# Kernel tuning notes

Measured on AMD Instinct MI355X. Metric: run time of the kernel, lower is better.

## Reference

```python
import jax, jax.numpy as jnp
import numpy as np

NUM_SEGMENTS = 16


def setup_inputs() -> dict:
    key = jax.random.key(0)
    k1, k2, k3 = jax.random.split(key, 3)
    x = jax.random.normal(k1, (8, 128, 512, 512), dtype=jnp.float32)
    conv_w = jax.random.normal(k2, (NUM_SEGMENTS, 1, 3, 3), dtype=jnp.float32) * (1.0 / 3.0)
    conv_b = jax.random.normal(k3, (NUM_SEGMENTS,), dtype=jnp.float32) * 0.1
    return {"x": x, "conv_w": conv_w, "conv_b": conv_b}


def reference(x, conv_w, conv_b):
    nseg = conv_w.shape[0]
    S = int(np.sqrt(nseg))  # size_segments (grid is S x S)
    B, C, H, W = x.shape
    ws = H // S  # tile side
    # L2 norm over channel dim, keepdim -> [B,1,H,W]
    l2 = jnp.sqrt(jnp.sum(x * x, axis=1, keepdims=True))
    # Extract S*S tiles in row-major (i,j) order -> [B, nseg, ws, ws]
    tiles = l2.reshape(B, S, ws, S, ws).transpose(0, 1, 3, 2, 4).reshape(B, nseg, ws, ws)
    # One distinct 3x3 conv (1->1 ch, pad 1) per tile == grouped conv with nseg groups
    y = jax.lax.conv_general_dilated(
        tiles, conv_w,
        window_strides=(1, 1), padding="SAME",
        feature_group_count=nseg,
        dimension_numbers=("NCHW", "OIHW", "NCHW"),
    )
    y = jax.nn.sigmoid(y + conv_b[None, :, None, None])
    # torch: chunk along channel, cat along dim=2 -> [B,1,nseg*ws,ws], then .view(l2.shape)
    return y.reshape(B, 1, nseg * ws, ws).reshape(B, 1, H, W)
```

## Files before the change

### kernel.cpp

```cpp
#include <hip/hip_runtime.h>
#include <math.h>

#define B_    8
#define C_    128
#define H_    512
#define W_    512
#define HW_   (H_ * W_)
#define NSEG_ 16
#define TS_   128
#define SGRID_ 4

__global__ __launch_bounds__(256) void l2norm_kernel(const float* __restrict__ x,
                                                     float* __restrict__ l2) {
    int t = blockIdx.x * blockDim.x + threadIdx.x;
    int q = t << 2;
    int b = q >> 18;
    int hw = q & (HW_ - 1);
    const float* p = x + (size_t)b * C_ * HW_ + hw;
    float s0 = 0.f, s1 = 0.f, s2 = 0.f, s3 = 0.f;
#pragma unroll 8
    for (int c = 0; c < C_; ++c) {
        float4 v = *reinterpret_cast<const float4*>(p + (size_t)c * HW_);
        s0 = fmaf(v.x, v.x, s0);
        s1 = fmaf(v.y, v.y, s1);
        s2 = fmaf(v.z, v.z, s2);
        s3 = fmaf(v.w, v.w, s3);
    }
    float4 r;
    r.x = sqrtf(s0); r.y = sqrtf(s1); r.z = sqrtf(s2); r.w = sqrtf(s3);
    *reinterpret_cast<float4*>(l2 + q) = r;
}

__global__ __launch_bounds__(256) void tileconv_kernel(const float* __restrict__ l2,
                                                       const float* __restrict__ w,
                                                       const float* __restrict__ bias,
                                                       float* __restrict__ out) {
    int t = blockIdx.x * blockDim.x + threadIdx.x;
    int c   = t & (TS_ - 1);
    int r   = (t >> 7) & (TS_ - 1);
    int seg = (t >> 14) & (NSEG_ - 1);
    int b   = t >> 18;
    int ti = seg >> 2;
    int tj = seg & 3;

    const float* wp = w + seg * 9;
    float w00 = wp[0], w01 = wp[1], w02 = wp[2];
    float w10 = wp[3], w11 = wp[4], w12 = wp[5];
    float w20 = wp[6], w21 = wp[7], w22 = wp[8];

    const float* base = l2 + (size_t)b * HW_ + (size_t)(ti * TS_) * W_ + tj * TS_;

    float acc = bias[seg];
    bool up = (r > 0), dn = (r < TS_ - 1);
    bool lf = (c > 0), rt = (c < TS_ - 1);

    const float* row0 = base + (r - 1) * W_ + c;
    const float* row1 = row0 + W_;
    const float* row2 = row1 + W_;

    if (up) {
        if (lf) acc = fmaf(row0[-1], w00, acc);
        acc = fmaf(row0[0], w01, acc);
        if (rt) acc = fmaf(row0[1], w02, acc);
    }
    if (lf) acc = fmaf(row1[-1], w10, acc);
    acc = fmaf(row1[0], w11, acc);
    if (rt) acc = fmaf(row1[1], w12, acc);
    if (dn) {
        if (lf) acc = fmaf(row2[-1], w20, acc);
        acc = fmaf(row2[0], w21, acc);
        if (rt) acc = fmaf(row2[1], w22, acc);
    }

    out[t] = 1.0f / (1.0f + expf(-acc));
}

extern "C" void kernel_launch(void* const* d_in, const int* in_sizes, int n_in,
                              void* d_out, int out_size, void* d_ws, size_t ws_size,
                              hipStream_t stream) {
    const float* x      = (const float*)d_in[0];
    const float* conv_w = (const float*)d_in[1];
    const float* conv_b = (const float*)d_in[2];
    float* out = (float*)d_out;
    float* l2  = (float*)d_ws;

    int n1 = B_ * HW_ / 4;
    l2norm_kernel<<<n1 / 256, 256, 0, stream>>>(x, l2);

    int n2 = B_ * NSEG_ * TS_ * TS_;
    tileconv_kernel<<<n2 / 256, 256, 0, stream>>>(l2, conv_w, conv_b, out);
}
```

Baseline: 1.327 ms.

## Fuse channel L2 norm and per-tile 3x3 conv into one kernel with LDS halo

Replaces the two-kernel pipeline with a single kernel. Each block computes the L2 norm for a 16-row strip of one tile plus a one-row halo, stores it in shared memory, and then applies the 3x3 conv and sigmoid from there. This removes the global l2 round trip and one launch. In exchange, halo rows are recomputed, which adds roughly 12% extra reads of the dominant 1 GiB input. Channel iteration starts at a block-dependent offset to stagger memory access.

```diff
diff --git a/kernel.cpp b/kernel.cpp
--- a/kernel.cpp
+++ b/kernel.cpp
@@ -1,78 +1,121 @@
 #include <hip/hip_runtime.h>
 #include <math.h>
 
-#define B_    8
-#define C_    128
-#define H_    512
-#define W_    512
-#define HW_   (H_ * W_)
-#define NSEG_ 16
-#define TS_   128
-#define SGRID_ 4
+#define B_     8
+#define C_     128
+#define H_     512
+#define W_     512
+#define HW_    (H_ * W_)
+#define NSEG_  16
+#define TS_    128
+#define R_     16
+#define LROWS_ (R_ + 2)
+#define LSTR_  136
 
-__global__ __launch_bounds__(256) void l2norm_kernel(const float* __restrict__ x,
-                                                     float* __restrict__ l2) {
-    int t = blockIdx.x * blockDim.x + threadIdx.x;
-    int q = t << 2;
-    int b = q >> 18;
-    int hw = q & (HW_ - 1);
-    const float* p = x + (size_t)b * C_ * HW_ + hw;
-    float s0 = 0.f, s1 = 0.f, s2 = 0.f, s3 = 0.f;
-#pragma unroll 8
-    for (int c = 0; c < C_; ++c) {
-        float4 v = *reinterpret_cast<const float4*>(p + (size_t)c * HW_);
-        s0 = fmaf(v.x, v.x, s0);
-        s1 = fmaf(v.y, v.y, s1);
-        s2 = fmaf(v.z, v.z, s2);
-        s3 = fmaf(v.w, v.w, s3);
-    }
-    float4 r;
-    r.x = sqrtf(s0); r.y = sqrtf(s1); r.z = sqrtf(s2); r.w = sqrtf(s3);
-    *reinterpret_cast<float4*>(l2 + q) = r;
-}
+__global__ __launch_bounds__(256) void fused_kernel(const float* __restrict__ x,
+                                                    const float* __restrict__ w,
+                                                    const float* __restrict__ bias,
+                                                    float* __restrict__ out) {
+    __shared__ float l2s[LROWS_][LSTR_];
 
-__global__ __launch_bounds__(256) void tileconv_kernel(const float* __restrict__ l2,
-                                                       const float* __restrict__ w,
-                                                       const float* __restrict__ bias,
-                                                       float* __restrict__ out) {
-    int t = blockIdx.x * blockDim.x + threadIdx.x;
-    int c   = t & (TS_ - 1);
-    int r   = (t >> 7) & (TS_ - 1);
-    int seg = (t >> 14) & (NSEG_ - 1);
-    int b   = t >> 18;
-    int ti = seg >> 2;
-    int tj = seg & 3;
+    const int tid = threadIdx.x;
+    const int blk = blockIdx.x;
+    const int s   = blk & 7;
+    const int seg = (blk >> 3) & (NSEG_ - 1);
+    const int b   = blk >> 7;
+    const int ti  = seg >> 2;
+    const int tj  = seg & 3;
 
     const float* wp = w + seg * 9;
-    float w00 = wp[0], w01 = wp[1], w02 = wp[2];
-    float w10 = wp[3], w11 = wp[4], w12 = wp[5];
-    float w20 = wp[6], w21 = wp[7], w22 = wp[8];
+    const float w00 = wp[0], w01 = wp[1], w02 = wp[2];
+    const float w10 = wp[3], w11 = wp[4], w12 = wp[5];
+    const float w20 = wp[6], w21 = wp[7], w22 = wp[8];
+    const float bb  = bias[seg];
 
-    const float* base = l2 + (size_t)b * HW_ + (size_t)(ti * TS_) * W_ + tj * TS_;
+    if (tid < LROWS_) { l2s[tid][3] = 0.f; l2s[tid][4 + TS_] = 0.f; }
 
-    float acc = bias[seg];
-    bool up = (r > 0), dn = (r < TS_ - 1);
-    bool lf = (c > 0), rt = (c < TS_ - 1);
+    const int p0 = tid, p1 = tid + 256, p2 = tid + 512;
+    const int rr0 = p0 >> 5, rr1 = p1 >> 5, rr2 = p2 >> 5;
+    const int c40 = p0 & 31, c41 = p1 & 31, c42 = p2 & 31;
+    const bool have2 = (tid < 64);
 
-    const float* row0 = base + (r - 1) * W_ + c;
-    const float* row1 = row0 + W_;
-    const float* row2 = row1 + W_;
+    const int ht0 = s * R_ + rr0 - 1;
+    const int ht1 = s * R_ + rr1 - 1;
+    const int ht2 = s * R_ + rr2 - 1;
+    const bool rv0 = (ht0 >= 0);
+    const bool rv2 = (ht2 <= TS_ - 1);
+    const int hc0 = rv0 ? ht0 : 0;
+    const int hc2 = rv2 ? ht2 : TS_ - 1;
 
-    if (up) {
-        if (lf) acc = fmaf(row0[-1], w00, acc);
-        acc = fmaf(row0[0], w01, acc);
-        if (rt) acc = fmaf(row0[1], w02, acc);
-    }
-    if (lf) acc = fmaf(row1[-1], w10, acc);
-    acc = fmaf(row1[0], w11, acc);
-    if (rt) acc = fmaf(row1[1], w12, acc);
-    if (dn) {
-        if (lf) acc = fmaf(row2[-1], w20, acc);
-        acc = fmaf(row2[0], w21, acc);
-        if (rt) acc = fmaf(row2[1], w22, acc);
+    const size_t bbase = (size_t)b * C_ * HW_;
+    const int wbase = tj * TS_;
+    const int c0 = blk & (C_ - 1);
+
+    const float* q0 = x + bbase + (size_t)c0 * HW_ + (size_t)(ti * TS_ + hc0) * W_ + wbase + c40 * 4;
+    const float* q1 = x + bbase + (size_t)c0 * HW_ + (size_t)(ti * TS_ + ht1) * W_ + wbase + c41 * 4;
+    const float* q2 = x + bbase + (size_t)c0 * HW_ + (size_t)(ti * TS_ + hc2) * W_ + wbase + c42 * 4;
+
+    float4 a0 = make_float4(0.f, 0.f, 0.f, 0.f);
+    float4 a1 = make_float4(0.f, 0.f, 0.f, 0.f);
+    float4 a2 = make_float4(0.f, 0.f, 0.f, 0.f);
+
+#define BODY                                                                      \
+    {                                                                             \
+        float4 v0 = *reinterpret_cast<const float4*>(q0); q0 += HW_;              \
+        a0.x = fmaf(v0.x, v0.x, a0.x); a0.y = fmaf(v0.y, v0.y, a0.y);             \
+        a0.z = fmaf(v0.z, v0.z, a0.z); a0.w = fmaf(v0.w, v0.w, a0.w);             \
+        float4 v1 = *reinterpret_cast<const float4*>(q1); q1 += HW_;              \
+        a1.x = fmaf(v1.x, v1.x, a1.x); a1.y = fmaf(v1.y, v1.y, a1.y);             \
+        a1.z = fmaf(v1.z, v1.z, a1.z); a1.w = fmaf(v1.w, v1.w, a1.w);             \
+        if (have2) {                                                              \
+            float4 v2 = *reinterpret_cast<const float4*>(q2);                     \
+            a2.x = fmaf(v2.x, v2.x, a2.x); a2.y = fmaf(v2.y, v2.y, a2.y);         \
+            a2.z = fmaf(v2.z, v2.z, a2.z); a2.w = fmaf(v2.w, v2.w, a2.w);         \
+        }                                                                         \
+        q2 += HW_;                                                                \
     }
 
-    out[t] = 1.0f / (1.0f + expf(-acc));
+    const int n1 = C_ - c0;
+#pragma unroll 4
+    for (int i = 0; i < n1; ++i) BODY
+    q0 -= (size_t)C_ * HW_;
+    q1 -= (size_t)C_ * HW_;
+    q2 -= (size_t)C_ * HW_;
+#pragma unroll 4
+    for (int i = 0; i < c0; ++i) BODY
+#undef BODY
+
+    float4 r0v, r1v;
+    if (rv0) r0v = make_float4(sqrtf(a0.x), sqrtf(a0.y), sqrtf(a0.z), sqrtf(a0.w));
+    else     r0v = make_float4(0.f, 0.f, 0.f, 0.f);
+    r1v = make_float4(sqrtf(a1.x), sqrtf(a1.y), sqrtf(a1.z), sqrtf(a1.w));
+    *reinterpret_cast<float4*>(&l2s[rr0][4 + c40 * 4]) = r0v;
+    *reinterpret_cast<float4*>(&l2s[rr1][4 + c41 * 4]) = r1v;
+    if (have2) {
+        float4 r2v;
+        if (rv2) r2v = make_float4(sqrtf(a2.x), sqrtf(a2.y), sqrtf(a2.z), sqrtf(a2.w));
+        else     r2v = make_float4(0.f, 0.f, 0.f, 0.f);
+        *reinterpret_cast<float4*>(&l2s[rr2][4 + c42 * 4]) = r2v;
+    }
+
+    __syncthreads();
+
+    const int c  = tid & (TS_ - 1);
+    const int r2 = tid >> 7;
+    float* op = out + (((size_t)(b * NSEG_ + seg)) << 14) + ((size_t)(s * R_) << 7) + c;
+
+#pragma unroll
+    for (int k = 0; k < 8; ++k) {
+        const int r = r2 + 2 * k;
+        const float* L0 = &l2s[r    ][3 + c];
+        const float* L1 = &l2s[r + 1][3 + c];
+        const float* L2 = &l2s[r + 2][3 + c];
+        float acc = bb;
+        acc = fmaf(L0[0], w00, acc); acc = fmaf(L0[1], w01, acc); acc = fmaf(L0[2], w02, acc);
+        acc = fmaf(L1[0], w10, acc); acc = fmaf(L1[1], w11, acc); acc = fmaf(L1[2], w12, acc);
+        acc = fmaf(L2[0], w20, acc); acc = fmaf(L2[1], w21, acc); acc = fmaf(L2[2], w22, acc);
+        op[(size_t)r << 7] = 1.0f / (1.0f + expf(-acc));
+    }
 }
 
 extern "C" void kernel_launch(void* const* d_in, const int* in_sizes, int n_in,
@@ -82,11 +125,6 @@
     const float* conv_w = (const float*)d_in[1];
     const float* conv_b = (const float*)d_in[2];
     float* out = (float*)d_out;
-    float* l2  = (float*)d_ws;
 
-    int n1 = B_ * HW_ / 4;
-    l2norm_kernel<<<n1 / 256, 256, 0, stream>>>(x, l2);
-
-    int n2 = B_ * NSEG_ * TS_ * TS_;
-    tileconv_kernel<<<n2 / 256, 256, 0, stream>>>(l2, conv_w, conv_b, out);
+    fused_kernel<<<B_ * NSEG_ * 8, 256, 0, stream>>>(x, conv_w, conv_b, out);
 }
```

Result: slower. 1.378 ms (+3.8%).

## Process more pixels per thread and stagger channel start across blocks in L2 norm

Applied to the files above, without the earlier changes.

The L2-norm kernel now gives each thread 16 pixels (four float4 loads per channel), launching 512 blocks instead of 2048. Each block starts its channel loop at a different offset (blockIdx mod C) and wraps around. The staggering is meant to spread concurrent accesses across memory channels and avoid blocks hitting the same channel planes at once, and the wider per-thread work adds memory-level parallelism. The cost is fewer resident waves on the GPU, which could leave bandwidth unused.

```diff
diff --git a/kernel.cpp b/kernel.cpp
--- a/kernel.cpp
+++ b/kernel.cpp
@@ -1,34 +1,73 @@
 #include <hip/hip_runtime.h>
 #include <math.h>
 
-#define B_    8
-#define C_    128
-#define H_    512
-#define W_    512
-#define HW_   (H_ * W_)
-#define NSEG_ 16
-#define TS_   128
+#define B_     8
+#define C_     128
+#define H_     512
+#define W_     512
+#define HW_    (H_ * W_)
+#define NSEG_  16
+#define TS_    128
 #define SGRID_ 4
 
 __global__ __launch_bounds__(256) void l2norm_kernel(const float* __restrict__ x,
                                                      float* __restrict__ l2) {
-    int t = blockIdx.x * blockDim.x + threadIdx.x;
-    int q = t << 2;
-    int b = q >> 18;
-    int hw = q & (HW_ - 1);
-    const float* p = x + (size_t)b * C_ * HW_ + hw;
-    float s0 = 0.f, s1 = 0.f, s2 = 0.f, s3 = 0.f;
-#pragma unroll 8
-    for (int c = 0; c < C_; ++c) {
-        float4 v = *reinterpret_cast<const float4*>(p + (size_t)c * HW_);
-        s0 = fmaf(v.x, v.x, s0);
-        s1 = fmaf(v.y, v.y, s1);
-        s2 = fmaf(v.z, v.z, s2);
-        s3 = fmaf(v.w, v.w, s3);
+    const int tid = threadIdx.x;
+    const int blk = blockIdx.x;
+    const int px0 = blk << 12;
+    const int b   = px0 >> 18;
+    const int hw  = px0 & (HW_ - 1);
+
+    const float* base = x + (size_t)b * C_ * HW_ + hw;
+
+    float4 a0 = make_float4(0.f, 0.f, 0.f, 0.f);
+    float4 a1 = make_float4(0.f, 0.f, 0.f, 0.f);
+    float4 a2 = make_float4(0.f, 0.f, 0.f, 0.f);
+    float4 a3 = make_float4(0.f, 0.f, 0.f, 0.f);
+
+    const int c0 = blk & (C_ - 1);
+    const float* p = base + (size_t)c0 * HW_;
+
+    const int o0 = tid << 2;
+    const int o1 = o0 + 1024;
+    const int o2 = o0 + 2048;
+    const int o3 = o0 + 3072;
+
+#define BODY                                                                   \
+    {                                                                          \
+        float4 v0 = *reinterpret_cast<const float4*>(p + o0);                  \
+        float4 v1 = *reinterpret_cast<const float4*>(p + o1);                  \
+        float4 v2 = *reinterpret_cast<const float4*>(p + o2);                  \
+        float4 v3 = *reinterpret_cast<const float4*>(p + o3);                  \
+        a0.x = fmaf(v0.x, v0.x, a0.x); a0.y = fmaf(v0.y, v0.y, a0.y);          \
+        a0.z = fmaf(v0.z, v0.z, a0.z); a0.w = fmaf(v0.w, v0.w, a0.w);          \
+        a1.x = fmaf(v1.x, v1.x, a1.x); a1.y = fmaf(v1.y, v1.y, a1.y);          \
+        a1.z = fmaf(v1.z, v1.z, a1.z); a1.w = fmaf(v1.w, v1.w, a1.w);          \
+        a2.x = fmaf(v2.x, v2.x, a2.x); a2.y = fmaf(v2.y, v2.y, a2.y);          \
+        a2.z = fmaf(v2.z, v2.z, a2.z); a2.w = fmaf(v2.w, v2.w, a2.w);          \
+        a3.x = fmaf(v3.x, v3.x, a3.x); a3.y = fmaf(v3.y, v3.y, a3.y);          \
+        a3.z = fmaf(v3.z, v3.z, a3.z); a3.w = fmaf(v3.w, v3.w, a3.w);          \
+        p += HW_;                                                              \
     }
+
+    const int n1 = C_ - c0;
+#pragma unroll 2
+    for (int i = 0; i < n1; ++i) BODY
+    p = base;
+#pragma unroll 2
+    for (int i = 0; i < c0; ++i) BODY
+#undef BODY
+
     float4 r;
-    r.x = sqrtf(s0); r.y = sqrtf(s1); r.z = sqrtf(s2); r.w = sqrtf(s3);
-    *reinterpret_cast<float4*>(l2 + q) = r;
+    float* o = l2 + px0;
+    r = make_float4(sqrtf(a0.x), sqrtf(a0.y), sqrtf(a0.z), sqrtf(a0.w));
+    *reinterpret_cast<float4*>(o + o0) = r;
+    r = make_float4(sqrtf(a1.x), sqrtf(a1.y), sqrtf(a1.z), sqrtf(a1.w));
+    *reinterpret_cast<float4*>(o + o1) = r;
+    r = make_float4(sqrtf(a2.x), sqrtf(a2.y), sqrtf(a2.z), sqrtf(a2.w));
+    *reinterpret_cast<float4*>(o + o2) = r;
+    r = make_float4(sqrtf(a3.x), sqrtf(a3.y), sqrtf(a3.z), sqrtf(a3.w));
+    *reinterpret_cast<float4*>(o + o3) = r;
 }
 
 __global__ __launch_bounds__(256) void tileconv_kernel(const float* __restrict__ l2,
@@ -84,8 +123,7 @@
     float* out = (float*)d_out;
     float* l2  = (float*)d_ws;
 
-    int n1 = B_ * HW_ / 4;
-    l2norm_kernel<<<n1 / 256, 256, 0, stream>>>(x, l2);
+    l2norm_kernel<<<512, 256, 0, stream>>>(x, l2);
 
     int n2 = B_ * NSEG_ * TS_ * TS_;
     tileconv_kernel<<<n2 / 256, 256, 0, stream>>>(l2, conv_w, conv_b, out);
```

After: 1.328 ms. Within noise of the previous version (+0.1%).
